# Performance work log

Hardware: AMD Instinct MI355X
Metric: run time of the kernel (lower is better)

The kernel has to match this reference:

```python
import jax, jax.numpy as jnp
import numpy as np

N = 50000        # nodes
E = 800000       # edges (avg degree 16)
NODE_D = 128     # node_attr_dim
EDGE_D = 16      # edge_attr_dim
HID = 300        # hidden_dim (module default)


def setup_inputs() -> dict:
    key = jax.random.key(0)
    ks = jax.random.split(key, 8)
    x = jax.random.normal(ks[0], (N, NODE_D), jnp.float32)
    edge_attr = jax.random.normal(ks[1], (E, EDGE_D), jnp.float32)
    edge_weight = jax.random.uniform(ks[2], (E,), jnp.float32)
    node_weight = jax.random.uniform(ks[3], (N,), jnp.float32)
    edge_index = jax.random.randint(ks[4], (2, E), 0, N, jnp.int32)
    # lin0: Linear(node_attr_dim + edge_attr_dim, hidden_dim)
    W0 = jax.random.normal(ks[5], (NODE_D + EDGE_D, HID), jnp.float32) / np.sqrt(NODE_D + EDGE_D)
    b0 = jnp.zeros((HID,), jnp.float32)
    # mp_layer.linear: Linear(hidden_dim, hidden_dim)
    W = jax.random.normal(ks[6], (HID, HID), jnp.float32) / np.sqrt(HID)
    b = jnp.zeros((HID,), jnp.float32)
    return dict(x=x, edge_attr=edge_attr, edge_weight=edge_weight,
                node_weight=node_weight, W0=W0, b0=b0, W=W, b=b,
                edge_index=edge_index)


def reference(x, edge_attr, edge_weight, node_weight, W0, b0, W, b, edge_index):
    src = edge_index[0]   # x_j (source, flow='source_to_target')
    dst = edge_index[1]   # aggregation target i
    n = x.shape[0]

    # --- isFirstLayer: weighted sum of incoming edge features, scattered at dst ---
    inc = jax.ops.segment_sum(edge_weight[:, None] * edge_attr, dst, num_segments=n)  # [N, EDGE_D]
    h0 = jax.nn.relu(jnp.concatenate([x, inc], axis=1) @ W0 + b0)                     # [N, HID]

    # --- MessagePassingLayer: message = edge_weight * x_j; aggr = mean at dst ---
    msg = edge_weight[:, None] * h0[src]                                              # [E, HID]
    agg = jax.ops.segment_sum(msg, dst, num_segments=n)                               # [N, HID]
    deg = jax.ops.segment_sum(jnp.ones((src.shape[0],), x.dtype), dst, num_segments=n)
    agg = agg / jnp.maximum(deg, 1.0)[:, None]  # scatter-mean (0 where no incoming edges)

    # --- update: relu(h0 + linear(aggr)) (add_residual=True) ---
    h = jax.nn.relu(h0 + agg @ W + b)
    # isLastLayer=False -> no node_weight scaling
    return (h, h0)
```

## Files before the change

kernel.cpp:

```cpp
#include <hip/hip_runtime.h>

#define NN 50000
#define NE 800000
#define ND 128
#define ED 16
#define HID 300
#define KP1 192
#define KP2 320
#define NP 320

#define SCAN_T 256
#define SCAN_B ((NN + SCAN_T - 1) / SCAN_T)

typedef __attribute__((ext_vector_type(8))) short short8;
typedef __attribute__((ext_vector_type(4))) float f32x4;

__device__ __forceinline__ unsigned short f2b(float f) {
    unsigned int u = __float_as_uint(f);
    u = (u + 0x7FFFu + ((u >> 16) & 1u)) >> 16;
    return (unsigned short)u;
}
__device__ __forceinline__ float blo(unsigned int u) {
    return __uint_as_float(u << 16);
}
__device__ __forceinline__ float bhi(unsigned int u) {
    return __uint_as_float(u & 0xffff0000u);
}

__device__ __forceinline__ void gload16(const void* g, void* l) {
    __builtin_amdgcn_global_load_lds(
        (const __attribute__((address_space(1))) void*)g,
        (__attribute__((address_space(3))) void*)l, 16, 0, 0);
}

__device__ __forceinline__ int block_iscan(int v, int tid) {
    int lane = tid & 63;
    #pragma unroll
    for (int off = 1; off < 64; off <<= 1) {
        int t = __shfl_up(v, off);
        if (lane >= off) v += t;
    }
    __shared__ int wsum[4];
    int wid = tid >> 6;
    if (lane == 63) wsum[wid] = v;
    __syncthreads();
    int add = 0;
    #pragma unroll
    for (int w = 0; w < 4; ++w)
        if (w < wid) add += wsum[w];
    return v + add;
}

__global__ void hist_kernel(const int* __restrict__ ei, int* __restrict__ rowptr) {
    int e4 = (blockIdx.x * blockDim.x + threadIdx.x) * 4;
    if (e4 < NE) {
        int4 d = *(const int4*)&ei[NE + e4];
        atomicAdd(&rowptr[d.x + 1], 1);
        atomicAdd(&rowptr[d.y + 1], 1);
        atomicAdd(&rowptr[d.z + 1], 1);
        atomicAdd(&rowptr[d.w + 1], 1);
    }
}

__global__ __launch_bounds__(SCAN_T) void scan1(int* __restrict__ rowptr,
                                                int* __restrict__ blockSums) {
    int i = blockIdx.x * SCAN_T + threadIdx.x;
    int v = (i < NN) ? rowptr[1 + i] : 0;
    v = block_iscan(v, threadIdx.x);
    if (i < NN) rowptr[1 + i] = v;
    if (threadIdx.x == SCAN_T - 1) blockSums[blockIdx.x] = v;
}

__global__ __launch_bounds__(SCAN_T) void scan2(int* __restrict__ blockSums) {
    int t = threadIdx.x;
    int orig = (t < SCAN_B) ? blockSums[t] : 0;
    int v = block_iscan(orig, t);
    if (t < SCAN_B) blockSums[t] = v - orig;
}

__global__ __launch_bounds__(SCAN_T) void scan3(int* __restrict__ rowptr,
                                                const int* __restrict__ blockSums,
                                                int* __restrict__ cursor) {
    int i = blockIdx.x * SCAN_T + threadIdx.x;
    if (i < NN) {
        int v = rowptr[1 + i] + blockSums[blockIdx.x];
        rowptr[1 + i] = v;
        if (i + 1 < NN) cursor[i + 1] = v;
    }
    if (i == 0) cursor[0] = 0;
}

__global__ void fill_kernel(const int* __restrict__ ei, const float* __restrict__ ew,
                            int* __restrict__ cursor, uint4* __restrict__ csr) {
    int e = blockIdx.x * blockDim.x + threadIdx.x;
    if (e < NE) {
        int d = ei[NE + e];
        int pos = atomicAdd(&cursor[d], 1);
        uint4 q;
        q.x = (unsigned int)ei[e];
        q.y = (unsigned int)e;
        q.z = __float_as_uint(ew[e]);
        q.w = 0;
        csr[pos] = q;
    }
}

__global__ __launch_bounds__(256) void prep_kernel(
    const float* __restrict__ x,
    const float* __restrict__ edge_attr,
    const int* __restrict__ rowptr,
    const uint4* __restrict__ csr,
    unsigned short* __restrict__ A1) {
    int n = (blockIdx.x * blockDim.x + threadIdx.x) >> 6;
    int lane = threadIdx.x & 63;
    if (n >= NN) return;

    float2 v = *(const float2*)&x[(size_t)n * ND + lane * 2];
    unsigned int o = (unsigned int)f2b(v.x) | ((unsigned int)f2b(v.y) << 16);
    *(unsigned int*)&A1[(size_t)n * KP1 + lane * 2] = o;

    int g = lane >> 4, j = lane & 15;
    int lo = rowptr[n], hi = rowptr[n + 1];
    float s = 0.f;
    for (int k = lo + g; k < hi; k += 16) {
        int k1 = (k + 4  < hi) ? k + 4  : k;
        int k2 = (k + 8  < hi) ? k + 8  : k;
        int k3 = (k + 12 < hi) ? k + 12 : k;
        uint4 e0 = csr[k],  e1 = csr[k1];
        uint4 e2 = csr[k2], e3 = csr[k3];
        float a0 = edge_attr[(size_t)e0.y * ED + j];
        float a1 = edge_attr[(size_t)e1.y * ED + j];
        float a2 = edge_attr[(size_t)e2.y * ED + j];
        float a3 = edge_attr[(size_t)e3.y * ED + j];
        s += __uint_as_float(e0.z) * a0;
        s += ((k + 4  < hi) ? __uint_as_float(e1.z) : 0.f) * a1;
        s += ((k + 8  < hi) ? __uint_as_float(e2.z) : 0.f) * a2;
        s += ((k + 12 < hi) ? __uint_as_float(e3.z) : 0.f) * a3;
    }
    s += __shfl_xor(s, 16);
    s += __shfl_xor(s, 32);
    if (lane < 16)
        A1[(size_t)n * KP1 + ND + lane] = f2b(s);
    else
        A1[(size_t)n * KP1 + ND + lane] = 0;
}

__global__ void castB0(const float* __restrict__ W0, unsigned short* __restrict__ B0T) {
    int n = blockIdx.x, k = threadIdx.x;
    float v = (n < HID && k < ND + ED) ? W0[(size_t)k * HID + n] : 0.f;
    B0T[(size_t)n * KP1 + k] = f2b(v);
}

__global__ void castB(const float* __restrict__ W, unsigned short* __restrict__ BT) {
    int n = blockIdx.x, k = threadIdx.x;
    float v = (n < HID && k < HID) ? W[(size_t)k * HID + n] : 0.f;
    BT[(size_t)n * KP2 + k] = f2b(v);
}

template <int MODE, int KP, int BN, int WM, int WN, int RPB, int NY>
__global__ __launch_bounds__(256) void gemm_stream(
    const unsigned short* __restrict__ A,
    const unsigned short* __restrict__ BT,
    const float* __restrict__ bias,
    const float* __restrict__ RES,
    float* __restrict__ C,
    unsigned short* __restrict__ h0b,
    int M)
{
    constexpr int CPR = KP / 8;
    constexpr int ACH = 32 * CPR;
    constexpr int BCH = BN * CPR;
    constexpr int AM  = 32 / (16 * WM);
    constexpr int BNW = BN / (16 * WN);
    __shared__ unsigned short Bs[BCH * 8];
    __shared__ unsigned short As[2][ACH * 8];

    const int tid = threadIdx.x;
    const int wave = tid >> 6, lane = tid & 63;
    const int wm = wave / WN, wn = wave % WN;
    const int quad = lane >> 4, lr = lane & 15;
    const int rbase = blockIdx.x * RPB;
    const int rowend = min(rbase + RPB, M);
    const int nt = (rowend - rbase + 31) >> 5;

    auto stageA = [&](int buf, int mb) {
        #pragma unroll
        for (int rd = 0; rd < ACH / 256; ++rd) {
            int s = rd * 256 + tid;
            int row = s / CPR, c = s - row * CPR;
            int cs = (c & ~7) | ((c & 7) ^ (row & 7));
            int mg = mb + row; if (mg >= M) mg = M - 1;
            gload16(&A[(size_t)mg * KP + cs * 8], &As[buf][s * 8]);
        }
    };

    #pragma unroll 1
    for (int ny = 0; ny < NY; ++ny) {
        const int n00 = ny * BN;
        const int ncol = n00 + wn * (BNW * 16);

        #pragma unroll
        for (int rd = 0; rd < BCH / 256; ++rd) {
            int s = rd * 256 + tid;
            int row = s / CPR, c = s - row * CPR;
            int cs = (c & ~7) | ((c & 7) ^ (row & 7));
            gload16(&BT[(size_t)(n00 + row) * KP + cs * 8], &Bs[s * 8]);
        }
        stageA(0, rbase);

        float bias_r[BNW];
        #pragma unroll
        for (int tn = 0; tn < BNW; ++tn) {
            int ng = ncol + tn * 16 + lr;
            bias_r[tn] = (ng < HID) ? bias[ng] : 0.f;
        }
        __syncthreads();

        int cur = 0;
        #pragma unroll 1
        for (int t = 0; t < nt; ++t) {
            const int mb = rbase + t * 32;
            if (t + 1 < nt) stageA(cur ^ 1, mb + 32);

            float res_r[AM][BNW][4];
            if (MODE == 1) {
                #pragma unroll
                for (int tm = 0; tm < AM; ++tm)
                #pragma unroll
                for (int tn = 0; tn < BNW; ++tn) {
                    int ng = ncol + tn * 16 + lr;
                    int ngc = ng < HID ? ng : HID - 1;
                    #pragma unroll
                    for (int r = 0; r < 4; ++r) {
                        int mg = mb + (wm * AM + tm) * 16 + quad * 4 + r;
                        int mgc = mg < M ? mg : M - 1;
                        res_r[tm][tn][r] = RES[(size_t)mgc * HID + ngc];
                    }
                }
            }

            f32x4 acc[AM][BNW] = {};
            const int rm = lr & 7;
            #pragma unroll
            for (int tt = 0; tt < KP / 32; ++tt) {
                int cA = tt * 4 + quad;
                int sw8 = ((cA & ~7) | ((cA & 7) ^ rm)) * 8;
                short8 a[AM], b[BNW];
                #pragma unroll
                for (int tm = 0; tm < AM; ++tm) {
                    int ar = (wm * AM + tm) * 16 + lr;
                    a[tm] = *(const short8*)&As[cur][ar * KP + sw8];
                }
                #pragma unroll
                for (int tn = 0; tn < BNW; ++tn) {
                    int br = wn * (BNW * 16) + tn * 16 + lr;
                    b[tn] = *(const short8*)&Bs[br * KP + sw8];
                }
                #pragma unroll
                for (int tm = 0; tm < AM; ++tm)
                    #pragma unroll
                    for (int tn = 0; tn < BNW; ++tn)
                        acc[tm][tn] = __builtin_amdgcn_mfma_f32_16x16x32_bf16(
                            a[tm], b[tn], acc[tm][tn], 0, 0, 0);
            }

            #pragma unroll
            for (int tm = 0; tm < AM; ++tm)
            #pragma unroll
            for (int tn = 0; tn < BNW; ++tn) {
                int ng = ncol + tn * 16 + lr;
                #pragma unroll
                for (int r = 0; r < 4; ++r) {
                    int mg = mb + (wm * AM + tm) * 16 + quad * 4 + r;
                    if (mg < rowend && ng < HID) {
                        float v = acc[tm][tn][r] + bias_r[tn];
                        if (MODE == 1) v += res_r[tm][tn][r];
                        v = fmaxf(v, 0.f);
                        C[(size_t)mg * HID + ng] = v;
                        if (MODE == 0) h0b[(size_t)mg * NP + ng] = f2b(v);
                    }
                }
            }
            __syncthreads();
            cur ^= 1;
        }
    }
}

__device__ __forceinline__ void acc8(float* acc, float w, const uint4& r) {
    acc[0] += w * blo(r.x); acc[1] += w * bhi(r.x);
    acc[2] += w * blo(r.y); acc[3] += w * bhi(r.y);
    acc[4] += w * blo(r.z); acc[5] += w * bhi(r.z);
    acc[6] += w * blo(r.w); acc[7] += w * bhi(r.w);
}

__global__ __launch_bounds__(256) void agg_kernel(
    const unsigned short* __restrict__ h0b,
    const int* __restrict__ rowptr,
    const uint4* __restrict__ csr,
    unsigned short* __restrict__ aggB)
{
    int n = (blockIdx.x * blockDim.x + threadIdx.x) >> 6;
    int lane = threadIdx.x & 63;
    if (n >= NN) return;
    int lo = rowptr[n], hi = rowptr[n + 1];
    float acc[8] = {};
    const uint4* h4 = (const uint4*)h0b;
    bool act = lane < 40;
    for (int k = lo; k < hi; k += 8) {
        uint4 p0 = csr[k];
        uint4 p1 = csr[(k + 1 < hi) ? k + 1 : k];
        uint4 p2 = csr[(k + 2 < hi) ? k + 2 : k];
        uint4 p3 = csr[(k + 3 < hi) ? k + 3 : k];
        uint4 p4 = csr[(k + 4 < hi) ? k + 4 : k];
        uint4 p5 = csr[(k + 5 < hi) ? k + 5 : k];
        uint4 p6 = csr[(k + 6 < hi) ? k + 6 : k];
        uint4 p7 = csr[(k + 7 < hi) ? k + 7 : k];
        float w0 = __uint_as_float(p0.z);
        float w1 = (k + 1 < hi) ? __uint_as_float(p1.z) : 0.f;
        float w2 = (k + 2 < hi) ? __uint_as_float(p2.z) : 0.f;
        float w3 = (k + 3 < hi) ? __uint_as_float(p3.z) : 0.f;
        float w4 = (k + 4 < hi) ? __uint_as_float(p4.z) : 0.f;
        float w5 = (k + 5 < hi) ? __uint_as_float(p5.z) : 0.f;
        float w6 = (k + 6 < hi) ? __uint_as_float(p6.z) : 0.f;
        float w7 = (k + 7 < hi) ? __uint_as_float(p7.z) : 0.f;
        uint4 r0 = {0,0,0,0}, r1 = {0,0,0,0}, r2 = {0,0,0,0}, r3 = {0,0,0,0};
        uint4 r4 = {0,0,0,0}, r5 = {0,0,0,0}, r6 = {0,0,0,0}, r7 = {0,0,0,0};
        if (act) {
            r0 = h4[(size_t)p0.x * 40 + lane];
            r1 = h4[(size_t)p1.x * 40 + lane];
            r2 = h4[(size_t)p2.x * 40 + lane];
            r3 = h4[(size_t)p3.x * 40 + lane];
            r4 = h4[(size_t)p4.x * 40 + lane];
            r5 = h4[(size_t)p5.x * 40 + lane];
            r6 = h4[(size_t)p6.x * 40 + lane];
            r7 = h4[(size_t)p7.x * 40 + lane];
        }
        acc8(acc, w0, r0); acc8(acc, w1, r1);
        acc8(acc, w2, r2); acc8(acc, w3, r3);
        acc8(acc, w4, r4); acc8(acc, w5, r5);
        acc8(acc, w6, r6); acc8(acc, w7, r7);
    }
    if (act) {
        float invd = 1.f / fmaxf((float)(hi - lo), 1.f);
        int cbase = lane * 8;
        unsigned int o[4];
        #pragma unroll
        for (int i = 0; i < 4; ++i) {
            int c0 = cbase + 2 * i, c1 = c0 + 1;
            unsigned int ulo = (c0 < HID) ? f2b(acc[2 * i] * invd) : 0;
            unsigned int uhi = (c1 < HID) ? f2b(acc[2 * i + 1] * invd) : 0;
            o[i] = ulo | (uhi << 16);
        }
        uint4* a4 = (uint4*)aggB;
        uint4 v; v.x = o[0]; v.y = o[1]; v.z = o[2]; v.w = o[3];
        a4[(size_t)n * 40 + lane] = v;
    }
}

extern "C" void kernel_launch(void* const* d_in, const int* in_sizes, int n_in,
                              void* d_out, int out_size, void* d_ws, size_t ws_size,
                              hipStream_t stream) {
    const float* x           = (const float*)d_in[0];
    const float* edge_attr   = (const float*)d_in[1];
    const float* edge_weight = (const float*)d_in[2];
    const float* W0 = (const float*)d_in[4];
    const float* b0 = (const float*)d_in[5];
    const float* W  = (const float*)d_in[6];
    const float* b  = (const float*)d_in[7];
    const int* ei   = (const int*)d_in[8];

    float* out = (float*)d_out;
    float* h  = out;
    float* h0 = out + (size_t)NN * HID;

    char* p = (char*)d_ws;
    auto alloc = [&](size_t bytes) { char* q = p; p += (bytes + 255) & ~(size_t)255; return q; };
    int*   rowptr  = (int*)  alloc((NN + 1) * sizeof(int));
    int*   cursor  = (int*)  alloc(NN * sizeof(int));
    int*   bsums   = (int*)  alloc(SCAN_B * sizeof(int));
    uint4* csr     = (uint4*)alloc((size_t)NE * sizeof(uint4));
    unsigned short* A1   = (unsigned short*)alloc((size_t)NN * KP1 * 2);
    unsigned short* h0b  = (unsigned short*)alloc((size_t)NN * NP * 2);
    unsigned short* aggB = (unsigned short*)alloc((size_t)NN * NP * 2);
    unsigned short* B0T  = (unsigned short*)alloc((size_t)NP * KP1 * 2);
    unsigned short* BT   = (unsigned short*)alloc((size_t)NP * KP2 * 2);

    hipMemsetAsync(rowptr, 0, (NN + 1) * sizeof(int), stream);
    hist_kernel<<<(NE / 4 + 255) / 256, 256, 0, stream>>>(ei, rowptr);
    scan1<<<SCAN_B, SCAN_T, 0, stream>>>(rowptr, bsums);
    scan2<<<1, SCAN_T, 0, stream>>>(bsums);
    scan3<<<SCAN_B, SCAN_T, 0, stream>>>(rowptr, bsums, cursor);
    fill_kernel<<<(NE + 255) / 256, 256, 0, stream>>>(ei, edge_weight, cursor, csr);
    castB0<<<NP, KP1, 0, stream>>>(W0, B0T);
    castB<<<NP, KP2, 0, stream>>>(W, BT);
    prep_kernel<<<(NN + 3) / 4, 256, 0, stream>>>(x, edge_attr, rowptr, csr, A1);

    gemm_stream<0, KP1, 320, 1, 4, 196, 1><<<dim3(256, 1), 256, 0, stream>>>(
        A1, B0T, b0, nullptr, h0, h0b, NN);
    agg_kernel<<<(NN + 3) / 4, 256, 0, stream>>>(h0b, rowptr, csr, aggB);
    gemm_stream<1, KP2, 160, 2, 2, 196, 2><<<dim3(256, 1), 256, 0, stream>>>(
        aggB, BT, b, h0, h, nullptr, NN);
}
```

Before: 457.7 us.

## Split GEMM N-tiles across grid.y, widen first GEMM to 512 threads, shrink gather unroll

The gemm_stream kernel no longer loops over N-tiles inside one block. The N-tile now comes from blockIdx.y, and the thread count becomes a template parameter. The first GEMM runs 8 waves (2x4) per block instead of 4. The second GEMM uses a 128x2 grid with twice the rows per block, so each block loads only half of B. The aggregation kernel's gather unroll drops from 8 to 4 edges to cut register pressure, which may reduce memory-level parallelism.

New measurement: 442.5 us. 3.3% less time.

```diff
diff --git a/kernel.cpp b/kernel.cpp
--- a/kernel.cpp
+++ b/kernel.cpp
@@ -157,8 +157,8 @@
     BT[(size_t)n * KP2 + k] = f2b(v);
 }
 
-template <int MODE, int KP, int BN, int WM, int WN, int RPB, int NY>
-__global__ __launch_bounds__(256) void gemm_stream(
+template <int MODE, int KP, int BN, int WM, int WN, int RPB, int THR>
+__global__ __launch_bounds__(THR) void gemm_stream(
     const unsigned short* __restrict__ A,
     const unsigned short* __restrict__ BT,
     const float* __restrict__ bias,
@@ -170,8 +170,10 @@
     constexpr int CPR = KP / 8;
     constexpr int ACH = 32 * CPR;
     constexpr int BCH = BN * CPR;
+    constexpr int NW  = THR / 64;
     constexpr int AM  = 32 / (16 * WM);
     constexpr int BNW = BN / (16 * WN);
+    static_assert(WM * WN == NW, "wave grid must cover block");
     __shared__ unsigned short Bs[BCH * 8];
     __shared__ unsigned short As[2][ACH * 8];
 
@@ -179,14 +181,14 @@
     const int wave = tid >> 6, lane = tid & 63;
     const int wm = wave / WN, wn = wave % WN;
     const int quad = lane >> 4, lr = lane & 15;
+    const int n00 = blockIdx.y * BN;
+    const int ncol = n00 + wn * (BNW * 16);
     const int rbase = blockIdx.x * RPB;
     const int rowend = min(rbase + RPB, M);
     const int nt = (rowend - rbase + 31) >> 5;
 
     auto stageA = [&](int buf, int mb) {
-        #pragma unroll
-        for (int rd = 0; rd < ACH / 256; ++rd) {
-            int s = rd * 256 + tid;
+        for (int s = tid; s < ACH; s += THR) {
             int row = s / CPR, c = s - row * CPR;
             int cs = (c & ~7) | ((c & 7) ^ (row & 7));
             int mg = mb + row; if (mg >= M) mg = M - 1;
@@ -194,96 +196,88 @@
         }
     };
 
+    for (int s = tid; s < BCH; s += THR) {
+        int row = s / CPR, c = s - row * CPR;
+        int cs = (c & ~7) | ((c & 7) ^ (row & 7));
+        gload16(&BT[(size_t)(n00 + row) * KP + cs * 8], &Bs[s * 8]);
+    }
+    stageA(0, rbase);
+
+    float bias_r[BNW];
+    #pragma unroll
+    for (int tn = 0; tn < BNW; ++tn) {
+        int ng = ncol + tn * 16 + lr;
+        bias_r[tn] = (ng < HID) ? bias[ng] : 0.f;
+    }
+    __syncthreads();
+
+    int cur = 0;
     #pragma unroll 1
-    for (int ny = 0; ny < NY; ++ny) {
-        const int n00 = ny * BN;
-        const int ncol = n00 + wn * (BNW * 16);
-
+    for (int t = 0; t < nt; ++t) {
+        const int mb = rbase + t * 32;
+        if (t + 1 < nt) stageA(cur ^ 1, mb + 32);
+
+        float res_r[AM][BNW][4];
+        if (MODE == 1) {
+            #pragma unroll
+            for (int tm = 0; tm < AM; ++tm)
+            #pragma unroll
+            for (int tn = 0; tn < BNW; ++tn) {
+                int ng = ncol + tn * 16 + lr;
+                int ngc = ng < HID ? ng : HID - 1;
+                #pragma unroll
+                for (int r = 0; r < 4; ++r) {
+                    int mg = mb + (wm * AM + tm) * 16 + quad * 4 + r;
+                    int mgc = mg < M ? mg : M - 1;
+                    res_r[tm][tn][r] = RES[(size_t)mgc * HID + ngc];
+                }
+            }
+        }
+
+        f32x4 acc[AM][BNW] = {};
+        const int rm = lr & 7;
         #pragma unroll
-        for (int rd = 0; rd < BCH / 256; ++rd) {
-            int s = rd * 256 + tid;
-            int row = s / CPR, c = s - row * CPR;
-            int cs = (c & ~7) | ((c & 7) ^ (row & 7));
-            gload16(&BT[(size_t)(n00 + row) * KP + cs * 8], &Bs[s * 8]);
-        }
-        stageA(0, rbase);
-
-        float bias_r[BNW];
+        for (int tt = 0; tt < KP / 32; ++tt) {
+            int cA = tt * 4 + quad;
+            int sw8 = ((cA & ~7) | ((cA & 7) ^ rm)) * 8;
+            short8 a[AM], b[BNW];
+            #pragma unroll
+            for (int tm = 0; tm < AM; ++tm) {
+                int ar = (wm * AM + tm) * 16 + lr;
+                a[tm] = *(const short8*)&As[cur][ar * KP + sw8];
+            }
+            #pragma unroll
+            for (int tn = 0; tn < BNW; ++tn) {
+                int br = wn * (BNW * 16) + tn * 16 + lr;
+                b[tn] = *(const short8*)&Bs[br * KP + sw8];
+            }
+            #pragma unroll
+            for (int tm = 0; tm < AM; ++tm)
+                #pragma unroll
+                for (int tn = 0; tn < BNW; ++tn)
+                    acc[tm][tn] = __builtin_amdgcn_mfma_f32_16x16x32_bf16(
+                        a[tm], b[tn], acc[tm][tn], 0, 0, 0);
+        }
+
+        #pragma unroll
+        for (int tm = 0; tm < AM; ++tm)
         #pragma unroll
         for (int tn = 0; tn < BNW; ++tn) {
             int ng = ncol + tn * 16 + lr;
-            bias_r[tn] = (ng < HID) ? bias[ng] : 0.f;
-        }
-        __syncthreads();
-
-        int cur = 0;
-        #pragma unroll 1
-        for (int t = 0; t < nt; ++t) {
-            const int mb = rbase + t * 32;
-            if (t + 1 < nt) stageA(cur ^ 1, mb + 32);
-
-            float res_r[AM][BNW][4];
-            if (MODE == 1) {
-                #pragma unroll
-                for (int tm = 0; tm < AM; ++tm)
-                #pragma unroll
-                for (int tn = 0; tn < BNW; ++tn) {
-                    int ng = ncol + tn * 16 + lr;
-                    int ngc = ng < HID ? ng : HID - 1;
-                    #pragma unroll
-                    for (int r = 0; r < 4; ++r) {
-                        int mg = mb + (wm * AM + tm) * 16 + quad * 4 + r;
-                        int mgc = mg < M ? mg : M - 1;
-                        res_r[tm][tn][r] = RES[(size_t)mgc * HID + ngc];
-                    }
+            #pragma unroll
+            for (int r = 0; r < 4; ++r) {
+                int mg = mb + (wm * AM + tm) * 16 + quad * 4 + r;
+                if (mg < rowend && ng < HID) {
+                    float v = acc[tm][tn][r] + bias_r[tn];
+                    if (MODE == 1) v += res_r[tm][tn][r];
+                    v = fmaxf(v, 0.f);
+                    C[(size_t)mg * HID + ng] = v;
+                    if (MODE == 0) h0b[(size_t)mg * NP + ng] = f2b(v);
                 }
             }
-
-            f32x4 acc[AM][BNW] = {};
-            const int rm = lr & 7;
-            #pragma unroll
-            for (int tt = 0; tt < KP / 32; ++tt) {
-                int cA = tt * 4 + quad;
-                int sw8 = ((cA & ~7) | ((cA & 7) ^ rm)) * 8;
-                short8 a[AM], b[BNW];
-                #pragma unroll
-                for (int tm = 0; tm < AM; ++tm) {
-                    int ar = (wm * AM + tm) * 16 + lr;
-                    a[tm] = *(const short8*)&As[cur][ar * KP + sw8];
-                }
-                #pragma unroll
-                for (int tn = 0; tn < BNW; ++tn) {
-                    int br = wn * (BNW * 16) + tn * 16 + lr;
-                    b[tn] = *(const short8*)&Bs[br * KP + sw8];
-                }
-                #pragma unroll
-                for (int tm = 0; tm < AM; ++tm)
-                    #pragma unroll
-                    for (int tn = 0; tn < BNW; ++tn)
-                        acc[tm][tn] = __builtin_amdgcn_mfma_f32_16x16x32_bf16(
-                            a[tm], b[tn], acc[tm][tn], 0, 0, 0);
-            }
-
-            #pragma unroll
-            for (int tm = 0; tm < AM; ++tm)
-            #pragma unroll
-            for (int tn = 0; tn < BNW; ++tn) {
-                int ng = ncol + tn * 16 + lr;
-                #pragma unroll
-                for (int r = 0; r < 4; ++r) {
-                    int mg = mb + (wm * AM + tm) * 16 + quad * 4 + r;
-                    if (mg < rowend && ng < HID) {
-                        float v = acc[tm][tn][r] + bias_r[tn];
-                        if (MODE == 1) v += res_r[tm][tn][r];
-                        v = fmaxf(v, 0.f);
-                        C[(size_t)mg * HID + ng] = v;
-                        if (MODE == 0) h0b[(size_t)mg * NP + ng] = f2b(v);
-                    }
-                }
-            }
-            __syncthreads();
-            cur ^= 1;
-        }
+        }
+        __syncthreads();
+        cur ^= 1;
     }
 }
 
@@ -307,39 +301,24 @@
     float acc[8] = {};
     const uint4* h4 = (const uint4*)h0b;
     bool act = lane < 40;
-    for (int k = lo; k < hi; k += 8) {
+    for (int k = lo; k < hi; k += 4) {
         uint4 p0 = csr[k];
         uint4 p1 = csr[(k + 1 < hi) ? k + 1 : k];
         uint4 p2 = csr[(k + 2 < hi) ? k + 2 : k];
         uint4 p3 = csr[(k + 3 < hi) ? k + 3 : k];
-        uint4 p4 = csr[(k + 4 < hi) ? k + 4 : k];
-        uint4 p5 = csr[(k + 5 < hi) ? k + 5 : k];
-        uint4 p6 = csr[(k + 6 < hi) ? k + 6 : k];
-        uint4 p7 = csr[(k + 7 < hi) ? k + 7 : k];
         float w0 = __uint_as_float(p0.z);
         float w1 = (k + 1 < hi) ? __uint_as_float(p1.z) : 0.f;
         float w2 = (k + 2 < hi) ? __uint_as_float(p2.z) : 0.f;
         float w3 = (k + 3 < hi) ? __uint_as_float(p3.z) : 0.f;
-        float w4 = (k + 4 < hi) ? __uint_as_float(p4.z) : 0.f;
-        float w5 = (k + 5 < hi) ? __uint_as_float(p5.z) : 0.f;
-        float w6 = (k + 6 < hi) ? __uint_as_float(p6.z) : 0.f;
-        float w7 = (k + 7 < hi) ? __uint_as_float(p7.z) : 0.f;
         uint4 r0 = {0,0,0,0}, r1 = {0,0,0,0}, r2 = {0,0,0,0}, r3 = {0,0,0,0};
-        uint4 r4 = {0,0,0,0}, r5 = {0,0,0,0}, r6 = {0,0,0,0}, r7 = {0,0,0,0};
         if (act) {
             r0 = h4[(size_t)p0.x * 40 + lane];
             r1 = h4[(size_t)p1.x * 40 + lane];
             r2 = h4[(size_t)p2.x * 40 + lane];
             r3 = h4[(size_t)p3.x * 40 + lane];
-            r4 = h4[(size_t)p4.x * 40 + lane];
-            r5 = h4[(size_t)p5.x * 40 + lane];
-            r6 = h4[(size_t)p6.x * 40 + lane];
-            r7 = h4[(size_t)p7.x * 40 + lane];
         }
         acc8(acc, w0, r0); acc8(acc, w1, r1);
         acc8(acc, w2, r2); acc8(acc, w3, r3);
-        acc8(acc, w4, r4); acc8(acc, w5, r5);
-        acc8(acc, w6, r6); acc8(acc, w7, r7);
     }
     if (act) {
         float invd = 1.f / fmaxf((float)(hi - lo), 1.f);
@@ -396,9 +375,9 @@
     castB<<<NP, KP2, 0, stream>>>(W, BT);
     prep_kernel<<<(NN + 3) / 4, 256, 0, stream>>>(x, edge_attr, rowptr, csr, A1);
 
-    gemm_stream<0, KP1, 320, 1, 4, 196, 1><<<dim3(256, 1), 256, 0, stream>>>(
+    gemm_stream<0, KP1, 320, 2, 4, 196, 512><<<dim3(256, 1), 512, 0, stream>>>(
         A1, B0T, b0, nullptr, h0, h0b, NN);
     agg_kernel<<<(NN + 3) / 4, 256, 0, stream>>>(h0b, rowptr, csr, aggB);
-    gemm_stream<1, KP2, 160, 2, 2, 196, 2><<<dim3(256, 1), 256, 0, stream>>>(
+    gemm_stream<1, KP2, 160, 2, 2, 391, 256><<<dim3(128, 2), 256, 0, stream>>>(
         aggB, BT, b, h0, h, nullptr, NN);
 }
```
